# Performance work log

Measured on AMD Instinct MI355X. Metric: run time of the kernel, lower is better.

The kernel has to match this reference:

```python
import jax, jax.numpy as jnp
import numpy as np

D_MODEL = 1024
SEL_DIM = 64
CONFIGS = [(4, 32), (8, 64), (16, 128)]  # (heads, dim)
B, T = 2, 2048


def setup_inputs() -> dict:
    key = jax.random.key(0)
    ks = jax.random.split(key, 20)
    s = 0.02  # init scale for stability
    inp = {
        "x": jax.random.normal(ks[0], (B, T, D_MODEL), jnp.float32),
        "sel_w1": jax.random.normal(ks[1], (SEL_DIM, D_MODEL), jnp.float32) * s,
        "sel_b1": jnp.zeros((SEL_DIM,), jnp.float32),
        "sel_w2": jax.random.normal(ks[2], (SEL_DIM, SEL_DIM), jnp.float32) * s,
        "sel_b2": jnp.zeros((SEL_DIM,), jnp.float32),
        "sel_w3": jax.random.normal(ks[3], (len(CONFIGS), SEL_DIM), jnp.float32) * s,
        "sel_b3": jnp.zeros((len(CONFIGS),), jnp.float32),
    }
    for i, (h, d) in enumerate(CONFIGS):
        inp[f"qw{i}"] = jax.random.normal(ks[4 + 3 * i], (h * d, D_MODEL), jnp.float32) * s
        inp[f"kw{i}"] = jax.random.normal(ks[5 + 3 * i], (d, D_MODEL), jnp.float32) * s
        inp[f"ww{i}"] = jax.random.normal(ks[6 + 3 * i], (h, D_MODEL), jnp.float32) * s
    return inp


def _seq_features(x):
    # x: [b,t,d]
    b, t, d = x.shape
    seq_mean = jnp.mean(x, axis=1, keepdims=True)            # [b,1,d]
    seq_std = jnp.std(x, axis=1, keepdims=True, ddof=1)      # torch.std is unbiased
    pos = (jnp.arange(t, dtype=x.dtype) / t)[None, :, None]  # [1,t,1] broadcast to [b,t,d]
    return x + seq_mean + seq_std + pos * 0.1


def _forward(x, sel_w1, sel_b1, sel_w2, sel_b2, sel_w3, sel_b3,
             qw0, kw0, ww0, qw1, kw1, ww1, qw2, kw2, ww2):
    b, t, dm = x.shape
    feats = _seq_features(x)
    h1 = jax.nn.relu(feats @ sel_w1.T + sel_b1)
    h2 = jax.nn.relu(h1 @ sel_w2.T + sel_b2)
    config_probs = jax.nn.softmax(h2 @ sel_w3.T + sel_b3, axis=-1)  # [b,t,ncfg]

    per_cfg = [(qw0, kw0, ww0), (qw1, kw1, ww1), (qw2, kw2, ww2)]
    final = jnp.zeros((b, t, t), dtype=x.dtype)
    for i, ((heads, dim), (qw, kw, ww)) in enumerate(zip(CONFIGS, per_cfg)):
        q = (x @ qw.T).reshape(b, t, heads, dim)   # [b,t,h,d]
        k = x @ kw.T                               # [b,s,d]
        w = x @ ww.T                               # [b,t,h]
        dots = jnp.einsum('bthd,bsd->bths', q, k)  # [b,t,h,s]
        score = jnp.einsum('bths,bth->bts', jax.nn.relu(dots), w)  # relu*weight, sum heads
        final = final + config_probs[:, :, i:i + 1] * score
    return final


def reference(x, sel_w1, sel_b1, sel_w2, sel_b2, sel_w3, sel_b3,
              qw0, kw0, ww0, qw1, kw1, ww1, qw2, kw2, ww2):
    return _forward(x, sel_w1, sel_b1, sel_w2, sel_b2, sel_w3, sel_b3,
                    qw0, kw0, ww0, qw1, kw1, ww1, qw2, kw2, ww2)
```

## Files before the change

### kernel.cpp

```cpp
#include <hip/hip_runtime.h>
#include <hip/hip_fp16.h>
#include <cstdint>
#include <cstddef>
#include <math.h>

#define B_ 2
#define T_ 2048
#define D_ 1024
#define M_ (B_*T_)

#define QO0 0
#define KO0 128
#define WO0 160
#define QO1 168
#define KO1 680
#define WO1 744
#define QO2 752
#define KO2 2800
#define WO2 2928
#define SELO 2944
#define LDN 3072

typedef float f32x16 __attribute__((ext_vector_type(16)));
typedef short bf16x8 __attribute__((ext_vector_type(8)));
typedef unsigned short u16;

__device__ __forceinline__ u16 f2bf(float f) {
    unsigned int u = __float_as_uint(f);
    unsigned int r = (u + 0x7fffu + ((u >> 16) & 1u)) >> 16;
    return (u16)r;
}
__device__ __forceinline__ float bf2f(u16 b) {
    return __uint_as_float(((unsigned int)b) << 16);
}

__device__ __forceinline__ void gload16(const void* g, void* l) {
    __builtin_amdgcn_global_load_lds(
        (const __attribute__((address_space(1))) unsigned int*)g,
        (__attribute__((address_space(3))) unsigned int*)l,
        16, 0, 0);
}

__device__ __forceinline__ void stage_plane(const u16* src_base, int row_stride, int k0,
                                            int rg, int lane, u16* dst) {
    int rl  = lane >> 2;
    int row = rg * 16 + rl;
    int q   = (lane & 3) ^ (rl & 3) ^ ((rl >> 2) & 3);
    const u16* s = src_base + (size_t)row * row_stride + k0 + q * 8;
    gload16(s, dst + rg * 512);
}

__global__ void stats1(const float* __restrict__ x, float* __restrict__ part,
                       float* __restrict__ part2, u16* __restrict__ Xh) {
    int d4 = threadIdx.x * 4;
    int tc = blockIdx.x;
    int b  = blockIdx.y;
    size_t base = (size_t)b * T_ * D_ + (size_t)tc * 16 * D_ + d4;
    float4 s = make_float4(0.f, 0.f, 0.f, 0.f);
    float4 s2 = make_float4(0.f, 0.f, 0.f, 0.f);
#pragma unroll
    for (int t = 0; t < 16; ++t) {
        float4 v = *(const float4*)(x + base + (size_t)t * D_);
        s.x += v.x; s.y += v.y; s.z += v.z; s.w += v.w;
        s2.x += v.x * v.x; s2.y += v.y * v.y; s2.z += v.z * v.z; s2.w += v.w * v.w;
        ushort4 h;
        h.x = f2bf(v.x); h.y = f2bf(v.y); h.z = f2bf(v.z); h.w = f2bf(v.w);
        *(ushort4*)(Xh + base + (size_t)t * D_) = h;
    }
    *(float4*)(part  + (size_t)(b * 128 + tc) * D_ + d4) = s;
    *(float4*)(part2 + (size_t)(b * 128 + tc) * D_ + d4) = s2;
}

__global__ void stats2(const float* __restrict__ part, const float* __restrict__ part2,
                       const float* __restrict__ w1,
                       float* __restrict__ msd, float* __restrict__ s1) {
    __shared__ float msL[1024];
    __shared__ float ps[64][17];
    __shared__ float pw[64][17];
    int b = blockIdx.x, tid = threadIdx.x;
    float s = 0.f, s2 = 0.f;
#pragma unroll 8
    for (int i = 0; i < 128; ++i) {
        s  += part [(b * 128 + i) * D_ + tid];
        s2 += part2[(b * 128 + i) * D_ + tid];
    }
    float mean = s / (float)T_;
    float var  = (s2 - (float)T_ * mean * mean) / (float)(T_ - 1);
    msL[tid] = mean + sqrtf(fmaxf(var, 0.f));
    __syncthreads();
    int j = tid >> 4, cc = tid & 15;
    float am = 0.f, aw = 0.f;
    const float* wr = w1 + (size_t)j * D_ + cc * 64;
    const float* mr = msL + cc * 64;
    for (int dd = 0; dd < 64; ++dd) { float w = wr[dd]; am += mr[dd] * w; aw += w; }
    ps[j][cc] = am; pw[j][cc] = aw;
    __syncthreads();
    if (tid < 64) {
        float sm = 0.f, sw = 0.f;
        for (int i = 0; i < 16; ++i) { sm += ps[tid][i]; sw += pw[tid][i]; }
        msd[b * 64 + tid] = sm;
        if (b == 0) s1[tid] = sw;
    }
}

__global__ void split_w(const float* __restrict__ qw0, const float* __restrict__ kw0,
                        const float* __restrict__ ww0, const float* __restrict__ qw1,
                        const float* __restrict__ kw1, const float* __restrict__ ww1,
                        const float* __restrict__ qw2, const float* __restrict__ kw2,
                        const float* __restrict__ ww2, const float* __restrict__ w1s,
                        u16* __restrict__ Wh) {
    int row = blockIdx.x;
    int col = threadIdx.x * 4;
    const float* src = nullptr;
    if      (row < 128)  src = qw0 + (size_t)row * D_;
    else if (row < 160)  src = kw0 + (size_t)(row - 128) * D_;
    else if (row < 164)  src = ww0 + (size_t)(row - 160) * D_;
    else if (row < 168)  src = nullptr;
    else if (row < 680)  src = qw1 + (size_t)(row - 168) * D_;
    else if (row < 744)  src = kw1 + (size_t)(row - 680) * D_;
    else if (row < 752)  src = ww1 + (size_t)(row - 744) * D_;
    else if (row < 2800) src = qw2 + (size_t)(row - 752) * D_;
    else if (row < 2928) src = kw2 + (size_t)(row - 2800) * D_;
    else if (row < 2944) src = ww2 + (size_t)(row - 2928) * D_;
    else if (row < 3008) src = w1s + (size_t)(row - 2944) * D_;
    float4 v = src ? *(const float4*)(src + col) : make_float4(0.f, 0.f, 0.f, 0.f);
    ushort4 h;
    h.x = f2bf(v.x); h.y = f2bf(v.y); h.z = f2bf(v.z); h.w = f2bf(v.w);
    *(ushort4*)&Wh[(size_t)row * D_ + col] = h;
}

__global__ __launch_bounds__(256, 3) void proj_gemm(
    const u16* __restrict__ Xh, const u16* __restrict__ Wh, u16* __restrict__ Ph) {
    __shared__ u16 As[8192], Bs[8192];
    int tid = threadIdx.x;
    int wave = tid >> 6, lane = tid & 63;
    int bm = blockIdx.x * 128, bn = blockIdx.y * 128;
    int wt = wave >> 1, wn = wave & 1;
    int fm = lane & 31, hv = lane >> 5;
    int tkey = (fm & 3) ^ ((fm >> 2) & 3);
    f32x16 acc[2][2];
#pragma unroll
    for (int i = 0; i < 2; ++i)
#pragma unroll
        for (int j = 0; j < 2; ++j)
#pragma unroll
            for (int r = 0; r < 16; ++r) acc[i][j][r] = 0.f;

    const u16* xh = Xh + (size_t)bm * D_;
    const u16* wh = Wh + (size_t)bn * D_;

    for (int kc = 0; kc < 16; ++kc) {
        int k0 = kc * 64;
#pragma unroll
        for (int i = 0; i < 8; ++i) {
            int j = wave * 8 + i;
            int mat = j >> 4;
            int pl  = (j >> 3) & 1;
            int rg  = j & 7;
            stage_plane(mat ? wh : xh, D_, k0 + pl * 32, rg, lane,
                        (mat ? Bs : As) + pl * 4096);
        }
        __syncthreads();
#pragma unroll
        for (int ks = 0; ks < 4; ++ks) {
            int pl = ks >> 1;
            int slot8 = (((ks & 1) * 2 + hv) ^ tkey) * 8;
            bf16x8 a_h[2], b_h[2];
#pragma unroll
            for (int t = 0; t < 2; ++t) {
                a_h[t] = *(const bf16x8*)&As[pl * 4096 + (wt * 64 + t * 32 + fm) * 32 + slot8];
                b_h[t] = *(const bf16x8*)&Bs[pl * 4096 + (wn * 64 + t * 32 + fm) * 32 + slot8];
            }
#pragma unroll
            for (int ti = 0; ti < 2; ++ti)
#pragma unroll
                for (int tj = 0; tj < 2; ++tj)
                    acc[ti][tj] = __builtin_amdgcn_mfma_f32_32x32x16_bf16(a_h[ti], b_h[tj], acc[ti][tj], 0, 0, 0);
        }
        __syncthreads();
    }
#pragma unroll
    for (int ti = 0; ti < 2; ++ti)
#pragma unroll
        for (int tj = 0; tj < 2; ++tj)
#pragma unroll
            for (int r = 0; r < 16; ++r) {
                int row = bm + wt * 64 + ti * 32 + (r & 3) + 8 * (r >> 2) + 4 * hv;
                int col = bn + wn * 64 + tj * 32 + fm;
                Ph[(size_t)row * LDN + col] = f2bf(acc[ti][tj][r]);
            }
}

__global__ void selector2(const u16* __restrict__ Ph,
                          const float* __restrict__ msd, const float* __restrict__ s1,
                          const float* __restrict__ b1, const float* __restrict__ w2,
                          const float* __restrict__ b2, const float* __restrict__ w3,
                          const float* __restrict__ b3, __half* __restrict__ WP) {
    __shared__ float h1s[4][64];
    __shared__ float h2s[4][64];
    __shared__ float lg[4][3];
    int tid = threadIdx.x;
    int slot = tid >> 6, j = tid & 63;
    int bt = blockIdx.x * 4 + slot;
    int b = bt >> 11, t = bt & 2047;
    size_t pidx = (size_t)bt * LDN + SELO + j;
    float v = bf2f(Ph[pidx])
            + msd[b * 64 + j] + 0.1f * ((float)t / (float)T_) * s1[j] + b1[j];
    h1s[slot][j] = fmaxf(v, 0.f);
    __syncthreads();
    float a2 = b2[j];
    {
        const float4* w2v = (const float4*)(w2 + (size_t)j * 64);
        const float4* h1v = (const float4*)h1s[slot];
#pragma unroll
        for (int d = 0; d < 16; ++d) {
            float4 wv = w2v[d], hv4 = h1v[d];
            a2 = fmaf(hv4.x, wv.x, a2);
            a2 = fmaf(hv4.y, wv.y, a2);
            a2 = fmaf(hv4.z, wv.z, a2);
            a2 = fmaf(hv4.w, wv.w, a2);
        }
    }
    h2s[slot][j] = fmaxf(a2, 0.f);
    __syncthreads();
    if (j < 3) {
        float a3 = b3[j];
        const float4* w3v = (const float4*)(w3 + (size_t)j * 64);
        const float4* h2v = (const float4*)h2s[slot];
#pragma unroll
        for (int d = 0; d < 16; ++d) {
            float4 wv = w3v[d], hv4 = h2v[d];
            a3 = fmaf(hv4.x, wv.x, a3);
            a3 = fmaf(hv4.y, wv.y, a3);
            a3 = fmaf(hv4.z, wv.z, a3);
            a3 = fmaf(hv4.w, wv.w, a3);
        }
        lg[slot][j] = a3;
    }
    __syncthreads();
    if (j < 28) {
        float m = fmaxf(lg[slot][0], fmaxf(lg[slot][1], lg[slot][2]));
        float e0 = expf(lg[slot][0] - m), e1 = expf(lg[slot][1] - m), e2 = expf(lg[slot][2] - m);
        float inv = 1.f / (e0 + e1 + e2);
        int wcol = (j < 4) ? (WO0 + j) : ((j < 12) ? (WO1 + j - 4) : (WO2 + j - 12));
        float p = ((j < 4) ? e0 : ((j < 12) ? e1 : e2)) * inv;
        float w = bf2f(Ph[(size_t)bt * LDN + wcol]);
        WP[(size_t)(b * 28 + j) * T_ + t] = __float2half(w * p);
    }
}

__device__ __forceinline__ int qcol_of(int c) {
    if (c < 2)  return QO0 + c * 64;
    if (c < 10) return QO1 + (c - 2) * 64;
    return QO2 + (c - 10) * 64;
}

__global__ __launch_bounds__(256, 2) void score_kernel(
    const u16* __restrict__ Ph, const __half* __restrict__ WP, float* __restrict__ out) {
    __shared__ u16 Qs[2][8192];
    __shared__ u16 Ks[4 * 4096];
    __shared__ __half wpL[3584];
    int tid = threadIdx.x;
    int wave = tid >> 6, lane = tid & 63;
    int wt = wave >> 1, wn = wave & 1;
    int fm = lane & 31, hv = lane >> 5;
    int tkey = (fm & 3) ^ ((fm >> 2) & 3);

    int n = blockIdx.z * 256 + blockIdx.y * 16 + blockIdx.x;
    int p = (n & 7) * 4 + (n >> 7);
    int xb = (n >> 3) & 15;
    int b = p >> 4, yb = p & 15;
    int t0 = yb * 128, s0 = xb * 128;

    const u16* Pq = Ph + (size_t)(b * T_ + t0) * LDN;
    const u16* Pk = Ph + (size_t)(b * T_ + s0) * LDN;

    auto stageQ = [&](int buf, int qcol) {
#pragma unroll
        for (int i = 0; i < 4; ++i) {
            int j = (wave << 2) + i;
            int pl = j >> 3, rg = j & 7;
            stage_plane(Pq, LDN, qcol + pl * 32, rg, lane, &Qs[buf][pl * 4096]);
        }
    };

#pragma unroll
    for (int i = 0; i < 6; ++i) {
        int j = i * 4 + wave;
        int pl = j >> 3, rg = j & 7;
        int col = (pl == 0) ? KO0 : ((pl == 1) ? KO1 : KO1 + 32);
        stage_plane(Pk, LDN, col, rg, lane, &Ks[pl * 4096]);
    }
#pragma unroll
    for (int i = 0; i < 2; ++i) {
        int j = i * 4 + wave;
        if (j < 7) {
            const __half* src = WP + (size_t)(b * 28 + j * 4 + (lane >> 4)) * T_ + t0 + (lane & 15) * 8;
            gload16(src, (u16*)wpL + j * 512);
        }
    }
    stageQ(0, QO0);

    f32x16 outacc[2][2], dots[2][2], Z16;
#pragma unroll
    for (int r = 0; r < 16; ++r) Z16[r] = 0.f;
#pragma unroll
    for (int i = 0; i < 2; ++i)
#pragma unroll
        for (int j = 0; j < 2; ++j)
#pragma unroll
            for (int r = 0; r < 16; ++r) { outacc[i][j][r] = 0.f; dots[i][j][r] = 0.f; }

    auto epi = [&](int g) {
#pragma unroll
        for (int ti = 0; ti < 2; ++ti) {
            int rowbase = wt * 64 + ti * 32 + 4 * hv;
#pragma unroll
            for (int rq = 0; rq < 4; ++rq) {
                __half2 wpq[2];
                *(short4*)wpq = *(const short4*)&wpL[g * 128 + rowbase + rq * 8];
                float2 f01 = __half22float2(wpq[0]);
                float2 f23 = __half22float2(wpq[1]);
                float wv[4] = {f01.x, f01.y, f23.x, f23.y};
#pragma unroll
                for (int tj = 0; tj < 2; ++tj)
#pragma unroll
                    for (int r2 = 0; r2 < 4; ++r2) {
                        int r = rq * 4 + r2;
                        outacc[ti][tj][r] += fmaxf(dots[ti][tj][r], 0.f) * wv[r2];
                    }
            }
        }
    };

    auto runPhase = [&](int c, int kpA, int kpB, bool z0, bool midBreak,
                        int gMid, bool hasEnd, int gEnd) {
        if (c + 1 < 42) {
            stageQ((c + 1) & 1, qcol_of(c + 1));
            asm volatile("s_waitcnt vmcnt(4)" ::: "memory");
        } else {
            asm volatile("s_waitcnt vmcnt(0)" ::: "memory");
        }
        __builtin_amdgcn_s_barrier();
        __builtin_amdgcn_sched_barrier(0);
        const u16* qb = Qs[c & 1];

        bf16x8 kf[2][2], qf[2][2];
        auto loadks = [&](int ks, int sl) {
            int kp = (ks < 2) ? kpA : kpB;
            int slot8 = (((ks & 1) * 2 + hv) ^ tkey) * 8;
#pragma unroll
            for (int tj = 0; tj < 2; ++tj)
                kf[sl][tj] = *(const bf16x8*)&Ks[kp * 4096 + (wn * 64 + tj * 32 + fm) * 32 + slot8];
#pragma unroll
            for (int ti = 0; ti < 2; ++ti)
                qf[sl][ti] = *(const bf16x8*)&qb[(ks >> 1) * 4096 + (wt * 64 + ti * 32 + fm) * 32 + slot8];
        };
        loadks(0, 0);
#pragma unroll
        for (int ks = 0; ks < 4; ++ks) {
            if (ks < 3) loadks(ks + 1, (ks + 1) & 1);
            bool zero = (ks == 0 && z0) || (ks == 2 && midBreak);
            int sl = ks & 1;
            __builtin_amdgcn_s_setprio(1);
#pragma unroll
            for (int ti = 0; ti < 2; ++ti)
#pragma unroll
                for (int tj = 0; tj < 2; ++tj)
                    dots[ti][tj] = __builtin_amdgcn_mfma_f32_32x32x16_bf16(
                        qf[sl][ti], kf[sl][tj], zero ? Z16 : dots[ti][tj], 0, 0, 0);
            __builtin_amdgcn_s_setprio(0);
            if (ks == 1 && midBreak) epi(gMid);
            if (ks == 3 && hasEnd)   epi(gEnd);
        }
        __builtin_amdgcn_sched_barrier(0);
        __builtin_amdgcn_s_barrier();
    };

#pragma unroll
    for (int c = 0; c < 2; ++c)
        runPhase(c, 0, 0, true, true, 2 * c, true, 2 * c + 1);
    for (int h = 0; h < 8; ++h) {
        runPhase(2 + h, 1, 2, true, false, -1, true, 4 + h);
        if (h == 7) {
            for (int j = wave; j < 32; j += 4) {
                int pl = j >> 3, rg = j & 7;
                stage_plane(Pk, LDN, KO2 + pl * 32, rg, lane, &Ks[pl * 4096]);
            }
        }
    }
    for (int h = 0; h < 16; ++h) {
        runPhase(10 + 2 * h, 0, 1, true, false, -1, false, -1);
        runPhase(11 + 2 * h, 2, 3, false, false, -1, true, 12 + h);
    }

#pragma unroll
    for (int ti = 0; ti < 2; ++ti)
#pragma unroll
        for (int tj = 0; tj < 2; ++tj)
#pragma unroll
            for (int r = 0; r < 16; ++r) {
                int trow = wt * 64 + ti * 32 + (r & 3) + 8 * (r >> 2) + 4 * hv;
                int scol = wn * 64 + tj * 32 + fm;
                __builtin_nontemporal_store(outacc[ti][tj][r],
                    &out[(size_t)(b * T_ + t0 + trow) * T_ + (s0 + scol)]);
            }
}

extern "C" void kernel_launch(void* const* d_in, const int* in_sizes, int n_in,
                              void* d_out, int out_size, void* d_ws, size_t ws_size,
                              hipStream_t stream) {
    const float* x   = (const float*)d_in[0];
    const float* w1  = (const float*)d_in[1];
    const float* b1  = (const float*)d_in[2];
    const float* w2  = (const float*)d_in[3];
    const float* b2  = (const float*)d_in[4];
    const float* w3  = (const float*)d_in[5];
    const float* b3  = (const float*)d_in[6];
    const float* qw0 = (const float*)d_in[7];
    const float* kw0 = (const float*)d_in[8];
    const float* ww0 = (const float*)d_in[9];
    const float* qw1 = (const float*)d_in[10];
    const float* kw1 = (const float*)d_in[11];
    const float* ww1 = (const float*)d_in[12];
    const float* qw2 = (const float*)d_in[13];
    const float* kw2 = (const float*)d_in[14];
    const float* ww2 = (const float*)d_in[15];
    float* out = (float*)d_out;

    float* fb = (float*)d_ws;
    float* PA  = fb; fb += (size_t)B_ * 128 * D_;
    float* PA2 = fb; fb += (size_t)B_ * 128 * D_;
    float* MSD = fb; fb += 128;
    float* S1  = fb; fb += 64;
    __half* WP = (__half*)fb; fb += (size_t)B_ * 28 * T_ / 2;
    u16* ub = (u16*)fb;
    u16* Wh = ub; ub += (size_t)LDN * D_;
    u16* Xh = ub; ub += (size_t)M_ * D_;
    u16* Ph = ub; ub += (size_t)M_ * LDN;

    stats1<<<dim3(128, B_), 256, 0, stream>>>(x, PA, PA2, Xh);
    stats2<<<dim3(B_), 1024, 0, stream>>>(PA, PA2, w1, MSD, S1);
    split_w<<<dim3(LDN), 256, 0, stream>>>(qw0, kw0, ww0, qw1, kw1, ww1,
                                           qw2, kw2, ww2, w1, Wh);
    proj_gemm<<<dim3(M_ / 128, LDN / 128), 256, 0, stream>>>(Xh, Wh, Ph);
    selector2<<<dim3(M_ / 4), 256, 0, stream>>>(Ph, MSD, S1, b1, w2, b2, w3, b3, WP);
    score_kernel<<<dim3(T_ / 128, T_ / 128, B_), 256, 0, stream>>>(Ph, WP, out);
}
```

Baseline: 256.4 us.

## Keep K fragments in registers, deepen Q staging ring, fuse prep kernels

The score kernel now loads every K plane (configs 0–2) into LDS once, copies the per-wave K fragments into registers, and reuses that space as a four-deep ring of Q buffers. Two Q phases are staged per barrier, which halves the number of barriers and removes repeated LDS reads of K. The stats1 and split_w kernels are merged into one prep launch to save a kernel launch. In exchange, holding 28 K fragments in VGPRs raises register pressure and may reduce occupancy or cause spills.

Measured after the change: 269.8 us. 5.2% more time.

```diff
diff --git a/kernel.cpp b/kernel.cpp
--- a/kernel.cpp
+++ b/kernel.cpp
@@ -50,25 +50,53 @@
     gload16(s, dst + rg * 512);
 }
 
-__global__ void stats1(const float* __restrict__ x, float* __restrict__ part,
-                       float* __restrict__ part2, u16* __restrict__ Xh) {
-    int d4 = threadIdx.x * 4;
-    int tc = blockIdx.x;
-    int b  = blockIdx.y;
-    size_t base = (size_t)b * T_ * D_ + (size_t)tc * 16 * D_ + d4;
-    float4 s = make_float4(0.f, 0.f, 0.f, 0.f);
-    float4 s2 = make_float4(0.f, 0.f, 0.f, 0.f);
-#pragma unroll
-    for (int t = 0; t < 16; ++t) {
-        float4 v = *(const float4*)(x + base + (size_t)t * D_);
-        s.x += v.x; s.y += v.y; s.z += v.z; s.w += v.w;
-        s2.x += v.x * v.x; s2.y += v.y * v.y; s2.z += v.z * v.z; s2.w += v.w * v.w;
+__global__ void prep(const float* __restrict__ x, float* __restrict__ part,
+                     float* __restrict__ part2, u16* __restrict__ Xh,
+                     const float* __restrict__ qw0, const float* __restrict__ kw0,
+                     const float* __restrict__ ww0, const float* __restrict__ qw1,
+                     const float* __restrict__ kw1, const float* __restrict__ ww1,
+                     const float* __restrict__ qw2, const float* __restrict__ kw2,
+                     const float* __restrict__ ww2, const float* __restrict__ w1s,
+                     u16* __restrict__ Wh) {
+    int bid = blockIdx.x;
+    if (bid < 256) {
+        int d4 = threadIdx.x * 4;
+        int tc = bid & 127;
+        int b  = bid >> 7;
+        size_t base = (size_t)b * T_ * D_ + (size_t)tc * 16 * D_ + d4;
+        float4 s = make_float4(0.f, 0.f, 0.f, 0.f);
+        float4 s2 = make_float4(0.f, 0.f, 0.f, 0.f);
+#pragma unroll
+        for (int t = 0; t < 16; ++t) {
+            float4 v = *(const float4*)(x + base + (size_t)t * D_);
+            s.x += v.x; s.y += v.y; s.z += v.z; s.w += v.w;
+            s2.x += v.x * v.x; s2.y += v.y * v.y; s2.z += v.z * v.z; s2.w += v.w * v.w;
+            ushort4 h;
+            h.x = f2bf(v.x); h.y = f2bf(v.y); h.z = f2bf(v.z); h.w = f2bf(v.w);
+            *(ushort4*)(Xh + base + (size_t)t * D_) = h;
+        }
+        *(float4*)(part  + (size_t)(b * 128 + tc) * D_ + d4) = s;
+        *(float4*)(part2 + (size_t)(b * 128 + tc) * D_ + d4) = s2;
+    } else {
+        int row = bid - 256;
+        int col = threadIdx.x * 4;
+        const float* src = nullptr;
+        if      (row < 128)  src = qw0 + (size_t)row * D_;
+        else if (row < 160)  src = kw0 + (size_t)(row - 128) * D_;
+        else if (row < 164)  src = ww0 + (size_t)(row - 160) * D_;
+        else if (row < 168)  src = nullptr;
+        else if (row < 680)  src = qw1 + (size_t)(row - 168) * D_;
+        else if (row < 744)  src = kw1 + (size_t)(row - 680) * D_;
+        else if (row < 752)  src = ww1 + (size_t)(row - 744) * D_;
+        else if (row < 2800) src = qw2 + (size_t)(row - 752) * D_;
+        else if (row < 2928) src = kw2 + (size_t)(row - 2800) * D_;
+        else if (row < 2944) src = ww2 + (size_t)(row - 2928) * D_;
+        else if (row < 3008) src = w1s + (size_t)(row - 2944) * D_;
+        float4 v = src ? *(const float4*)(src + col) : make_float4(0.f, 0.f, 0.f, 0.f);
         ushort4 h;
         h.x = f2bf(v.x); h.y = f2bf(v.y); h.z = f2bf(v.z); h.w = f2bf(v.w);
-        *(ushort4*)(Xh + base + (size_t)t * D_) = h;
-    }
-    *(float4*)(part  + (size_t)(b * 128 + tc) * D_ + d4) = s;
-    *(float4*)(part2 + (size_t)(b * 128 + tc) * D_ + d4) = s2;
+        *(ushort4*)&Wh[(size_t)row * D_ + col] = h;
+    }
 }
 
 __global__ void stats2(const float* __restrict__ part, const float* __restrict__ part2,
@@ -101,32 +129,6 @@
         msd[b * 64 + tid] = sm;
         if (b == 0) s1[tid] = sw;
     }
-}
-
-__global__ void split_w(const float* __restrict__ qw0, const float* __restrict__ kw0,
-                        const float* __restrict__ ww0, const float* __restrict__ qw1,
-                        const float* __restrict__ kw1, const float* __restrict__ ww1,
-                        const float* __restrict__ qw2, const float* __restrict__ kw2,
-                        const float* __restrict__ ww2, const float* __restrict__ w1s,
-                        u16* __restrict__ Wh) {
-    int row = blockIdx.x;
-    int col = threadIdx.x * 4;
-    const float* src = nullptr;
-    if      (row < 128)  src = qw0 + (size_t)row * D_;
-    else if (row < 160)  src = kw0 + (size_t)(row - 128) * D_;
-    else if (row < 164)  src = ww0 + (size_t)(row - 160) * D_;
-    else if (row < 168)  src = nullptr;
-    else if (row < 680)  src = qw1 + (size_t)(row - 168) * D_;
-    else if (row < 744)  src = kw1 + (size_t)(row - 680) * D_;
-    else if (row < 752)  src = ww1 + (size_t)(row - 744) * D_;
-    else if (row < 2800) src = qw2 + (size_t)(row - 752) * D_;
-    else if (row < 2928) src = kw2 + (size_t)(row - 2800) * D_;
-    else if (row < 2944) src = ww2 + (size_t)(row - 2928) * D_;
-    else if (row < 3008) src = w1s + (size_t)(row - 2944) * D_;
-    float4 v = src ? *(const float4*)(src + col) : make_float4(0.f, 0.f, 0.f, 0.f);
-    ushort4 h;
-    h.x = f2bf(v.x); h.y = f2bf(v.y); h.z = f2bf(v.z); h.w = f2bf(v.w);
-    *(ushort4*)&Wh[(size_t)row * D_ + col] = h;
 }
 
 __global__ __launch_bounds__(256, 3) void proj_gemm(
@@ -257,9 +259,9 @@
 
 __global__ __launch_bounds__(256, 2) void score_kernel(
     const u16* __restrict__ Ph, const __half* __restrict__ WP, float* __restrict__ out) {
-    __shared__ u16 Qs[2][8192];
-    __shared__ u16 Ks[4 * 4096];
+    __shared__ u16 Qr[4][8192];
     __shared__ __half wpL[3584];
+    u16* QrF = &Qr[0][0];
     int tid = threadIdx.x;
     int wave = tid >> 6, lane = tid & 63;
     int wt = wave >> 1, wn = wave & 1;
@@ -274,22 +276,35 @@
 
     const u16* Pq = Ph + (size_t)(b * T_ + t0) * LDN;
     const u16* Pk = Ph + (size_t)(b * T_ + s0) * LDN;
-
-    auto stageQ = [&](int buf, int qcol) {
+    int rl = lane >> 2;
+    int q8 = ((lane & 3) ^ (rl & 3) ^ ((rl >> 2) & 3)) * 8;
+    const u16* PqL = Pq + (size_t)rl * LDN + q8;
+    const u16* PkL = Pk + (size_t)rl * LDN + q8;
+
+    auto stageQ = [&](u16* buf, int qcol) {
 #pragma unroll
         for (int i = 0; i < 4; ++i) {
             int j = (wave << 2) + i;
             int pl = j >> 3, rg = j & 7;
-            stage_plane(Pq, LDN, qcol + pl * 32, rg, lane, &Qs[buf][pl * 4096]);
+            gload16(PqL + (size_t)(rg * 16) * LDN + pl * 32 + qcol,
+                    buf + pl * 4096 + rg * 512);
         }
     };
 
 #pragma unroll
-    for (int i = 0; i < 6; ++i) {
+    for (int i = 0; i < 14; ++i) {
         int j = i * 4 + wave;
-        int pl = j >> 3, rg = j & 7;
-        int col = (pl == 0) ? KO0 : ((pl == 1) ? KO1 : KO1 + 32);
-        stage_plane(Pk, LDN, col, rg, lane, &Ks[pl * 4096]);
+        int rg, col, offW;
+        if (j < 24) {
+            int pl = j >> 3; rg = j & 7;
+            col = (pl == 0) ? KO0 : ((pl == 1) ? KO1 : KO1 + 32);
+            offW = 16384 + pl * 4096;
+        } else {
+            int jj = j - 24; int pl = jj >> 3; rg = jj & 7;
+            col = KO2 + pl * 32;
+            offW = pl * 4096;
+        }
+        gload16(PkL + (size_t)(rg * 16) * LDN + col, QrF + offW + rg * 512);
     }
 #pragma unroll
     for (int i = 0; i < 2; ++i) {
@@ -299,7 +314,34 @@
             gload16(src, (u16*)wpL + j * 512);
         }
     }
-    stageQ(0, QO0);
+    __syncthreads();
+
+    int slotE = (hv ^ tkey) * 8;
+    int slotO = (((2 + hv)) ^ tkey) * 8;
+    int rowK0 = (wn * 64 + fm) * 32;
+    int rowK1 = rowK0 + 32 * 32;
+    bf16x8 krE[7][2], krO[7][2];
+#pragma unroll
+    for (int pp = 0; pp < 7; ++pp) {
+        int base = (pp < 3) ? (16384 + pp * 4096) : ((pp - 3) * 4096);
+        krE[pp][0] = *(const bf16x8*)(QrF + base + rowK0 + slotE);
+        krE[pp][1] = *(const bf16x8*)(QrF + base + rowK1 + slotE);
+        krO[pp][0] = *(const bf16x8*)(QrF + base + rowK0 + slotO);
+        krO[pp][1] = *(const bf16x8*)(QrF + base + rowK1 + slotO);
+    }
+    asm volatile("s_waitcnt lgkmcnt(0)" ::: "memory");
+    __syncthreads();
+
+    stageQ(QrF,         qcol_of(0));
+    stageQ(QrF +  8192, qcol_of(1));
+    stageQ(QrF + 16384, qcol_of(2));
+    stageQ(QrF + 24576, qcol_of(3));
+    __syncthreads();
+
+    int qoE0 = (wt * 64 + fm) * 32 + slotE;
+    int qoE1 = qoE0 + 32 * 32;
+    int qoO0 = (wt * 64 + fm) * 32 + slotO;
+    int qoO1 = qoO0 + 32 * 32;
 
     f32x16 outacc[2][2], dots[2][2], Z16;
 #pragma unroll
@@ -333,65 +375,91 @@
         }
     };
 
-    auto runPhase = [&](int c, int kpA, int kpB, bool z0, bool midBreak,
-                        int gMid, bool hasEnd, int gEnd) {
-        if (c + 1 < 42) {
-            stageQ((c + 1) & 1, qcol_of(c + 1));
-            asm volatile("s_waitcnt vmcnt(4)" ::: "memory");
+    auto MFMA4 = [&](bf16x8 q0, bf16x8 q1, bf16x8 k0, bf16x8 k1, bool zero) {
+        __builtin_amdgcn_s_setprio(1);
+        dots[0][0] = __builtin_amdgcn_mfma_f32_32x32x16_bf16(q0, k0, zero ? Z16 : dots[0][0], 0, 0, 0);
+        dots[0][1] = __builtin_amdgcn_mfma_f32_32x32x16_bf16(q0, k1, zero ? Z16 : dots[0][1], 0, 0, 0);
+        dots[1][0] = __builtin_amdgcn_mfma_f32_32x32x16_bf16(q1, k0, zero ? Z16 : dots[1][0], 0, 0, 0);
+        dots[1][1] = __builtin_amdgcn_mfma_f32_32x32x16_bf16(q1, k1, zero ? Z16 : dots[1][1], 0, 0, 0);
+        __builtin_amdgcn_s_setprio(0);
+    };
+
+    auto computePhase = [&](const u16* qb,
+                            bf16x8 kEa0, bf16x8 kEa1, bf16x8 kOa0, bf16x8 kOa1,
+                            bf16x8 kEb0, bf16x8 kEb1, bf16x8 kOb0, bf16x8 kOb1,
+                            bool z0, bool midBreak, int gMid, bool hasEnd, int gEnd) {
+        bf16x8 q0 = *(const bf16x8*)(qb + qoE0);
+        bf16x8 q1 = *(const bf16x8*)(qb + qoE1);
+        bf16x8 n0, n1;
+        n0 = *(const bf16x8*)(qb + qoO0);
+        n1 = *(const bf16x8*)(qb + qoO1);
+        MFMA4(q0, q1, kEa0, kEa1, z0);
+        q0 = n0; q1 = n1;
+        n0 = *(const bf16x8*)(qb + 4096 + qoE0);
+        n1 = *(const bf16x8*)(qb + 4096 + qoE1);
+        MFMA4(q0, q1, kOa0, kOa1, false);
+        if (midBreak) epi(gMid);
+        q0 = n0; q1 = n1;
+        n0 = *(const bf16x8*)(qb + 4096 + qoO0);
+        n1 = *(const bf16x8*)(qb + 4096 + qoO1);
+        MFMA4(q0, q1, kEb0, kEb1, midBreak);
+        q0 = n0; q1 = n1;
+        MFMA4(q0, q1, kOb0, kOb1, false);
+        if (hasEnd) epi(gEnd);
+    };
+
+    computePhase(QrF,        krE[0][0], krE[0][1], krO[0][0], krO[0][1],
+                             krE[0][0], krE[0][1], krO[0][0], krO[0][1],
+                 true, true, 0, true, 1);
+    computePhase(QrF + 8192, krE[0][0], krE[0][1], krO[0][0], krO[0][1],
+                             krE[0][0], krE[0][1], krO[0][0], krO[0][1],
+                 true, true, 2, true, 3);
+    asm volatile("s_waitcnt lgkmcnt(0)" ::: "memory");
+    __builtin_amdgcn_sched_barrier(0);
+    __builtin_amdgcn_s_barrier();
+
+    for (int e = 1; e <= 4; ++e) {
+        int c0 = 2 * e;
+        stageQ(QrF + ((c0 + 2) & 3) * 8192, qcol_of(c0 + 2));
+        stageQ(QrF + ((c0 + 3) & 3) * 8192, qcol_of(c0 + 3));
+        asm volatile("s_waitcnt vmcnt(8)" ::: "memory");
+        __builtin_amdgcn_s_barrier();
+        __builtin_amdgcn_sched_barrier(0);
+        computePhase(QrF + (c0 & 3) * 8192,
+                     krE[1][0], krE[1][1], krO[1][0], krO[1][1],
+                     krE[2][0], krE[2][1], krO[2][0], krO[2][1],
+                     true, false, -1, true, c0 + 2);
+        computePhase(QrF + ((c0 + 1) & 3) * 8192,
+                     krE[1][0], krE[1][1], krO[1][0], krO[1][1],
+                     krE[2][0], krE[2][1], krO[2][0], krO[2][1],
+                     true, false, -1, true, c0 + 3);
+        asm volatile("s_waitcnt lgkmcnt(0)" ::: "memory");
+        __builtin_amdgcn_sched_barrier(0);
+        __builtin_amdgcn_s_barrier();
+    }
+
+    for (int e = 5; e <= 20; ++e) {
+        int c0 = 2 * e;
+        if (e < 20) {
+            stageQ(QrF + ((c0 + 2) & 3) * 8192, qcol_of(c0 + 2));
+            stageQ(QrF + ((c0 + 3) & 3) * 8192, qcol_of(c0 + 3));
+            asm volatile("s_waitcnt vmcnt(8)" ::: "memory");
         } else {
             asm volatile("s_waitcnt vmcnt(0)" ::: "memory");
         }
         __builtin_amdgcn_s_barrier();
         __builtin_amdgcn_sched_barrier(0);
-        const u16* qb = Qs[c & 1];
-
-        bf16x8 kf[2][2], qf[2][2];
-        auto loadks = [&](int ks, int sl) {
-            int kp = (ks < 2) ? kpA : kpB;
-            int slot8 = (((ks & 1) * 2 + hv) ^ tkey) * 8;
-#pragma unroll
-            for (int tj = 0; tj < 2; ++tj)
-                kf[sl][tj] = *(const bf16x8*)&Ks[kp * 4096 + (wn * 64 + tj * 32 + fm) * 32 + slot8];
-#pragma unroll
-            for (int ti = 0; ti < 2; ++ti)
-                qf[sl][ti] = *(const bf16x8*)&qb[(ks >> 1) * 4096 + (wt * 64 + ti * 32 + fm) * 32 + slot8];
-        };
-        loadks(0, 0);
-#pragma unroll
-        for (int ks = 0; ks < 4; ++ks) {
-            if (ks < 3) loadks(ks + 1, (ks + 1) & 1);
-            bool zero = (ks == 0 && z0) || (ks == 2 && midBreak);
-            int sl = ks & 1;
-            __builtin_amdgcn_s_setprio(1);
-#pragma unroll
-            for (int ti = 0; ti < 2; ++ti)
-#pragma unroll
-                for (int tj = 0; tj < 2; ++tj)
-                    dots[ti][tj] = __builtin_amdgcn_mfma_f32_32x32x16_bf16(
-                        qf[sl][ti], kf[sl][tj], zero ? Z16 : dots[ti][tj], 0, 0, 0);
-            __builtin_amdgcn_s_setprio(0);
-            if (ks == 1 && midBreak) epi(gMid);
-            if (ks == 3 && hasEnd)   epi(gEnd);
-        }
+        computePhase(QrF + (c0 & 3) * 8192,
+                     krE[3][0], krE[3][1], krO[3][0], krO[3][1],
+                     krE[4][0], krE[4][1], krO[4][0], krO[4][1],
+                     true, false, -1, false, -1);
+        computePhase(QrF + ((c0 + 1) & 3) * 8192,
+                     krE[5][0], krE[5][1], krO[5][0], krO[5][1],
+                     krE[6][0], krE[6][1], krO[6][0], krO[6][1],
+                     false, false, -1, true, 12 + (e - 5));
+        asm volatile("s_waitcnt lgkmcnt(0)" ::: "memory");
         __builtin_amdgcn_sched_barrier(0);
         __builtin_amdgcn_s_barrier();
-    };
-
-#pragma unroll
-    for (int c = 0; c < 2; ++c)
-        runPhase(c, 0, 0, true, true, 2 * c, true, 2 * c + 1);
-    for (int h = 0; h < 8; ++h) {
-        runPhase(2 + h, 1, 2, true, false, -1, true, 4 + h);
-        if (h == 7) {
-            for (int j = wave; j < 32; j += 4) {
-                int pl = j >> 3, rg = j & 7;
-                stage_plane(Pk, LDN, KO2 + pl * 32, rg, lane, &Ks[pl * 4096]);
-            }
-        }
-    }
-    for (int h = 0; h < 16; ++h) {
-        runPhase(10 + 2 * h, 0, 1, true, false, -1, false, -1);
-        runPhase(11 + 2 * h, 2, 3, false, false, -1, true, 12 + h);
     }
 
 #pragma unroll
@@ -439,10 +507,10 @@
     u16* Xh = ub; ub += (size_t)M_ * D_;
     u16* Ph = ub; ub += (size_t)M_ * LDN;
 
-    stats1<<<dim3(128, B_), 256, 0, stream>>>(x, PA, PA2, Xh);
+    prep<<<dim3(256 + LDN), 256, 0, stream>>>(x, PA, PA2, Xh,
+                                              qw0, kw0, ww0, qw1, kw1, ww1,
+                                              qw2, kw2, ww2, w1, Wh);
     stats2<<<dim3(B_), 1024, 0, stream>>>(PA, PA2, w1, MSD, S1);
-    split_w<<<dim3(LDN), 256, 0, stream>>>(qw0, kw0, ww0, qw1, kw1, ww1,
-                                           qw2, kw2, ww2, w1, Wh);
     proj_gemm<<<dim3(M_ / 128, LDN / 128), 256, 0, stream>>>(Xh, Wh, Ph);
     selector2<<<dim3(M_ / 4), 256, 0, stream>>>(Ph, MSD, S1, b1, w2, b2, w3, b3, WP);
     score_kernel<<<dim3(T_ / 128, T_ / 128, B_), 256, 0, stream>>>(Ph, WP, out);
```
